# Kernel tuning notes

Measured on AMD Instinct MI355X. Metric: run time of the kernel, lower is better.

The kernel has to match this reference:

```python
import jax, jax.numpy as jnp
import numpy as np

IN_NC = 512

def setup_inputs() -> dict:
    key = jax.random.key(0)
    k1, k2, k3, k4 = jax.random.split(key, 4)
    B, N = 8, 2048
    nd, out_nc = 512, 512
    x = jax.random.normal(k1, (B, N * IN_NC), dtype=jnp.float32)
    # store weights as [in_nc, d] so projection is x @ W (same math as torch Linear with W^T)
    Wq = jax.random.normal(k2, (IN_NC, nd), dtype=jnp.float32) * (1.0 / np.sqrt(IN_NC))
    Wk = jax.random.normal(k3, (IN_NC, nd), dtype=jnp.float32) * (1.0 / np.sqrt(IN_NC))
    Wv = jax.random.normal(k4, (IN_NC, out_nc), dtype=jnp.float32) * (1.0 / np.sqrt(IN_NC))
    return {"x": x, "Wq": Wq, "Wk": Wk, "Wv": Wv}

def reference(x, Wq, Wk, Wv):
    B = x.shape[0]
    N = x.shape[1] // IN_NC
    xt = x.reshape(B, N, IN_NC)                     # [B, N, in_nc]
    Q = jnp.einsum('bnc,cd->bnd', xt, Wq)           # [B, N, nd]
    K = jnp.einsum('bnc,cd->bnd', xt, Wk)           # [B, N, nd]
    V = jnp.einsum('bnc,cd->bnd', xt, Wv)           # [B, N, out_nc]
    A = jnp.einsum('bnd,bmd->bnm', Q, K)            # [B, N, N]  (no scale, as in source)
    A = jax.nn.softmax(A, axis=-1)
    out = jnp.einsum('bnm,bmd->bnd', A, V)          # [B, N, out_nc]
    return out.reshape(B, -1)
```

## Files before the change

### kernel.cpp

```cpp
#include <hip/hip_runtime.h>
#include <hip/hip_fp16.h>

typedef _Float16 f16x8 __attribute__((ext_vector_type(8)));
typedef _Float16 f16x4 __attribute__((ext_vector_type(4)));
typedef float    f32x4 __attribute__((ext_vector_type(4)));

#define LOG2E 1.44269504f

__device__ __forceinline__ void stage128x64(const _Float16* __restrict__ g, int ld,
                                            void* lds, int tid)
{
    const int r0   = tid >> 3;
    const int colh = ((tid & 7) ^ (r0 & 7)) << 3;
    char* lbase = (char*)lds + (tid >> 6) * 1024;
#pragma unroll
    for (int i = 0; i < 4; i++) {
        const _Float16* src = g + (size_t)(i * 32 + r0) * ld + colh;
        __builtin_amdgcn_global_load_lds(
            (const __attribute__((address_space(1))) void*)src,
            (__attribute__((address_space(3))) void*)(lbase + i * 4096),
            16, 0, 0);
    }
}

__device__ __forceinline__ f16x8 lds_frag(const void* lds, int row, int colh)
{
    const int off = row * 128 + ((colh * 2) ^ ((row & 7) << 4));
    return *(const f16x8*)((const char*)lds + off);
}

__device__ __forceinline__ void mfma_tile(const void* a_lds, const void* b_lds,
                                          f32x4 acc[4][4],
                                          int wr, int wc, int lrow, int lkg)
{
#pragma unroll
    for (int kk = 0; kk < 2; kk++) {
        f16x8 af[4], bf[4];
#pragma unroll
        for (int mi = 0; mi < 4; mi++)
            af[mi] = lds_frag(a_lds, wr * 64 + mi * 16 + lrow, kk * 32 + lkg * 8);
#pragma unroll
        for (int ni = 0; ni < 4; ni++)
            bf[ni] = lds_frag(b_lds, wc * 64 + ni * 16 + lrow, kk * 32 + lkg * 8);
#pragma unroll
        for (int mi = 0; mi < 4; mi++)
#pragma unroll
            for (int ni = 0; ni < 4; ni++)
                acc[mi][ni] = __builtin_amdgcn_mfma_f32_16x16x32_f16(af[mi], bf[ni], acc[mi][ni], 0, 0, 0);
    }
}

__device__ __forceinline__ void gemm_loop_db(const _Float16* __restrict__ A, int lda,
                                             const _Float16* __restrict__ B, int ldb,
                                             int nk,
                                             _Float16* a0, _Float16* a1,
                                             _Float16* b0, _Float16* b1,
                                             f32x4 acc[4][4], int tid,
                                             int wr, int wc, int lrow, int lkg)
{
    stage128x64(A, lda, a0, tid);
    stage128x64(B, ldb, b0, tid);
    __syncthreads();
    for (int t = 0; t < nk; ++t) {
        _Float16* acur = (t & 1) ? a1 : a0;
        _Float16* bcur = (t & 1) ? b1 : b0;
        if (t + 1 < nk) {
            _Float16* anx = (t & 1) ? a0 : a1;
            _Float16* bnx = (t & 1) ? b0 : b1;
            stage128x64(A + (size_t)(t + 1) * 64, lda, anx, tid);
            stage128x64(B + (size_t)(t + 1) * 64, ldb, bnx, tid);
        }
        mfma_tile(acur, bcur, acc, wr, wc, lrow, lkg);
        __syncthreads();
    }
}

__global__ __launch_bounds__(256)
void convert_kernel(const float* __restrict__ x,
                    const float* __restrict__ Wq,
                    const float* __restrict__ Wk,
                    const float* __restrict__ Wv,
                    _Float16* __restrict__ xh,
                    _Float16* __restrict__ Wt)
{
    const int b = blockIdx.x;
    if (b < 2048) {
        const size_t base = (size_t)b * 4096 + (size_t)threadIdx.x * 4;
#pragma unroll
        for (int i = 0; i < 4; i++) {
            f32x4 v = *(const f32x4*)(x + base + i * 1024);
            f16x4 h;
#pragma unroll
            for (int j = 0; j < 4; j++) h[j] = (_Float16)v[j];
            *(f16x4*)(xh + base + i * 1024) = h;
        }
    } else {
        __shared__ float tb[32][33];
        const int t = b - 2048;
        const int mat = t >> 8;
        const int tile = t & 255;
        const int tr = tile >> 4, tc = tile & 15;
        const float* W = (mat == 0) ? Wq : (mat == 1) ? Wk : Wv;
        const int r = threadIdx.x >> 5, c = threadIdx.x & 31;
#pragma unroll
        for (int p = 0; p < 4; p++)
            tb[p * 8 + r][c] = W[(size_t)(tr * 32 + p * 8 + r) * 512 + tc * 32 + c];
        __syncthreads();
#pragma unroll
        for (int p = 0; p < 4; p++)
            Wt[((size_t)mat * 512 + tc * 32 + p * 8 + r) * 512 + tr * 32 + c] =
                (_Float16)tb[c][p * 8 + r];
    }
}

__global__ __launch_bounds__(256)
void proj_kernel(const _Float16* __restrict__ xh,
                 const _Float16* __restrict__ Wt,
                 _Float16* __restrict__ Qf,
                 _Float16* __restrict__ Kf,
                 _Float16* __restrict__ Vt)
{
    __shared__ _Float16 a0[128 * 64], a1[128 * 64];
    __shared__ _Float16 b0[128 * 64], b1[128 * 64];

    const int tid = threadIdx.x;
    const int mb = blockIdx.x, cb = blockIdx.y;
    const int mat = cb >> 2, nb = cb & 3;
    const int m0 = mb * 128, n0 = nb * 128;

    const _Float16* Abase = xh + (size_t)m0 * 512;
    const _Float16* Bbase = Wt + ((size_t)mat * 512 + n0) * 512;

    const int lane = tid & 63;
    const int w = tid >> 6;
    const int wr = w >> 1, wc = w & 1;
    const int lrow = lane & 15, lkg = lane >> 4;

    f32x4 acc[4][4];
#pragma unroll
    for (int i = 0; i < 4; i++)
#pragma unroll
        for (int j = 0; j < 4; j++) acc[i][j] = (f32x4)0.0f;

    gemm_loop_db(Abase, 512, Bbase, 512, 8, a0, a1, b0, b1,
                 acc, tid, wr, wc, lrow, lkg);

    if (mat < 2) {
        _Float16* Out = (mat == 0) ? Qf : Kf;
#pragma unroll
        for (int mi = 0; mi < 4; mi++) {
            const int mbase = m0 + wr * 64 + mi * 16 + lkg * 4;
#pragma unroll
            for (int ni = 0; ni < 4; ni++) {
                const int ncol = n0 + wc * 64 + ni * 16 + lrow;
#pragma unroll
                for (int r = 0; r < 4; r++)
                    Out[(size_t)(mbase + r) * 512 + ncol] = (_Float16)acc[mi][ni][r];
            }
        }
    } else {
#pragma unroll
        for (int mi = 0; mi < 4; mi++) {
            const int mglob = m0 + wr * 64 + mi * 16 + lkg * 4;
            const int b = mglob >> 11, mloc = mglob & 2047;
#pragma unroll
            for (int ni = 0; ni < 4; ni++) {
                const int d = n0 + wc * 64 + ni * 16 + lrow;
                f16x4 h;
#pragma unroll
                for (int r = 0; r < 4; r++) h[r] = (_Float16)acc[mi][ni][r];
                *(f16x4*)&Vt[((size_t)b * 512 + d) * 2048 + mloc] = h;
            }
        }
    }
}

__global__ __launch_bounds__(256)
void score_kernel(const _Float16* __restrict__ Qf,
                  const _Float16* __restrict__ Kf,
                  _Float16* __restrict__ P,
                  float2* __restrict__ ML, int b0)
{
    __shared__ __align__(16) char smem[65536];
    _Float16* a0 = (_Float16*)smem;
    _Float16* a1 = (_Float16*)(smem + 16384);
    _Float16* b0p = (_Float16*)(smem + 32768);
    _Float16* b1p = (_Float16*)(smem + 49152);
    float (*S_lds)[132] = (float(*)[132])smem;

    const int tid = threadIdx.x;
    const int mb = blockIdx.x, nb = blockIdx.y, bl = blockIdx.z;
    const int bg = b0 + bl;

    const _Float16* Abase = Qf + (size_t)(bg * 2048 + nb * 128) * 512;
    const _Float16* Bbase = Kf + (size_t)(bg * 2048 + mb * 128) * 512;

    const int lane = tid & 63;
    const int w = tid >> 6;
    const int wr = w >> 1, wc = w & 1;
    const int lrow = lane & 15, lkg = lane >> 4;

    f32x4 acc[4][4];
#pragma unroll
    for (int i = 0; i < 4; i++)
#pragma unroll
        for (int j = 0; j < 4; j++) acc[i][j] = (f32x4)0.0f;

    gemm_loop_db(Abase, 512, Bbase, 512, 8, a0, a1, b0p, b1p,
                 acc, tid, wr, wc, lrow, lkg);

    _Float16* Pb = P + (size_t)bl * 2048 * 2048;
    const int s  = tid >> 2;
    const int c0 = (tid & 3) * 32;

#pragma unroll
    for (int hp = 0; hp < 2; hp++) {
#pragma unroll
        for (int m2 = 0; m2 < 2; m2++) {
            const int mi = hp * 2 + m2;
            const int srow = wr * 32 + m2 * 16 + lkg * 4;
#pragma unroll
            for (int ni = 0; ni < 4; ni++) {
                const int col = wc * 64 + ni * 16 + lrow;
#pragma unroll
                for (int rr = 0; rr < 4; rr++)
                    S_lds[srow + rr][col] = acc[mi][ni][rr];
            }
        }
        __syncthreads();

        f32x4 vv[8];
#pragma unroll
        for (int j = 0; j < 8; j++)
            vv[j] = *(const f32x4*)&S_lds[s][c0 + j * 4];

        float m = vv[0][0];
#pragma unroll
        for (int j = 0; j < 8; j++)
#pragma unroll
            for (int jj = 0; jj < 4; jj++) m = fmaxf(m, vv[j][jj]);
        m = fmaxf(m, __shfl_xor(m, 1));
        m = fmaxf(m, __shfl_xor(m, 2));

        float l = 0.0f;
#pragma unroll
        for (int j = 0; j < 8; j++)
#pragma unroll
            for (int jj = 0; jj < 4; jj++) {
                float e = exp2f((vv[j][jj] - m) * LOG2E);
                vv[j][jj] = e;
                l += e;
            }
        l += __shfl_xor(l, 1);
        l += __shfl_xor(l, 2);

        const int q_local = (s >> 5) * 64 + hp * 32 + (s & 31);
        const int q = nb * 128 + q_local;

        if ((tid & 3) == 0) {
            float2 v; v.x = m; v.y = l;
            ML[((size_t)bl * 2048 + q) * 16 + mb] = v;
        }

#pragma unroll
        for (int j = 0; j < 4; j++) {
            f16x8 h;
#pragma unroll
            for (int jj = 0; jj < 8; jj++) {
                const int idx = j * 8 + jj;
                h[jj] = (_Float16)vv[idx >> 2][idx & 3];
            }
            *(f16x8*)&Pb[(size_t)q * 2048 + mb * 128 + c0 + j * 8] = h;
        }
        __syncthreads();
    }
}

__global__ __launch_bounds__(256)
void out_kernel(const _Float16* __restrict__ P,
                const _Float16* __restrict__ Vt,
                const float2* __restrict__ ML,
                float* __restrict__ out, int b0)
{
    __shared__ _Float16 a0[128 * 64], a1[128 * 64];
    __shared__ _Float16 b0p[128 * 64], b1p[128 * 64];
    __shared__ float scale_lds[128][17];

    const int tid = threadIdx.x;
    const int db = blockIdx.x >> 4, nb = blockIdx.x & 15, bl = blockIdx.y;
    const int bg = b0 + bl;

    if (tid < 128) {
        const float2* mlrow = ML + ((size_t)bl * 2048 + nb * 128 + tid) * 16;
        float2 ml[16];
        float M = -3.4e38f;
#pragma unroll
        for (int t = 0; t < 16; t++) { ml[t] = mlrow[t]; M = fmaxf(M, ml[t].x); }
        float L = 0.0f;
#pragma unroll
        for (int t = 0; t < 16; t++) L += ml[t].y * exp2f((ml[t].x - M) * LOG2E);
        const float invL = 1.0f / L;
#pragma unroll
        for (int t = 0; t < 16; t++)
            scale_lds[tid][t] = exp2f((ml[t].x - M) * LOG2E) * invL;
    }

    const _Float16* Abase = P  + (size_t)bl * 2048 * 2048 + (size_t)(nb * 128) * 2048;
    const _Float16* Bbase = Vt + (size_t)bg * 512  * 2048 + (size_t)(db * 128) * 2048;

    const int lane = tid & 63;
    const int w = tid >> 6;
    const int wr = w >> 1, wc = w & 1;
    const int lrow = lane & 15, lkg = lane >> 4;

    f32x4 acc[4][4];
#pragma unroll
    for (int i = 0; i < 4; i++)
#pragma unroll
        for (int j = 0; j < 4; j++) acc[i][j] = (f32x4)0.0f;

    stage128x64(Abase, 2048, a0, tid);
    stage128x64(Bbase, 2048, b0p, tid);
    __syncthreads();

    for (int t = 0; t < 32; ++t) {
        _Float16* acur = (t & 1) ? a1 : a0;
        _Float16* bcur = (t & 1) ? b1p : b0p;
        if (t + 1 < 32) {
            _Float16* anx = (t & 1) ? a0 : a1;
            _Float16* bnx = (t & 1) ? b0p : b1p;
            stage128x64(Abase + (size_t)(t + 1) * 64, 2048, anx, tid);
            stage128x64(Bbase + (size_t)(t + 1) * 64, 2048, bnx, tid);
        }
        const int kt = t >> 1;
#pragma unroll
        for (int kk = 0; kk < 2; kk++) {
            f16x8 af[4], bf[4];
#pragma unroll
            for (int mi = 0; mi < 4; mi++) {
                af[mi] = lds_frag(acur, wr * 64 + mi * 16 + lrow, kk * 32 + lkg * 8);
                const _Float16 hs = (_Float16)scale_lds[wr * 64 + mi * 16 + lrow][kt];
                af[mi] *= hs;
            }
#pragma unroll
            for (int ni = 0; ni < 4; ni++)
                bf[ni] = lds_frag(bcur, wc * 64 + ni * 16 + lrow, kk * 32 + lkg * 8);
#pragma unroll
            for (int mi = 0; mi < 4; mi++)
#pragma unroll
                for (int ni = 0; ni < 4; ni++)
                    acc[mi][ni] = __builtin_amdgcn_mfma_f32_16x16x32_f16(af[mi], bf[ni], acc[mi][ni], 0, 0, 0);
        }
        __syncthreads();
    }

#pragma unroll
    for (int mi = 0; mi < 4; mi++) {
        const int nbase = nb * 128 + wr * 64 + mi * 16 + lkg * 4;
#pragma unroll
        for (int ni = 0; ni < 4; ni++) {
            const int d = db * 128 + wc * 64 + ni * 16 + lrow;
#pragma unroll
            for (int rr = 0; rr < 4; rr++)
                out[((size_t)bg * 2048 + nbase + rr) * 512 + d] = acc[mi][ni][rr];
        }
    }
}

extern "C" void kernel_launch(void* const* d_in, const int* in_sizes, int n_in,
                              void* d_out, int out_size, void* d_ws, size_t ws_size,
                              hipStream_t stream) {
    const float* x  = (const float*)d_in[0];
    const float* Wq = (const float*)d_in[1];
    const float* Wk = (const float*)d_in[2];
    const float* Wv = (const float*)d_in[3];

    const size_t MB = 1024ull * 1024ull;
    char* ws = (char*)d_ws;
    _Float16* Qf = (_Float16*)ws;
    _Float16* Kf = Qf + (size_t)16384 * 512;
    _Float16* Vt = Kf + (size_t)16384 * 512;
    _Float16* P  = Vt + (size_t)16384 * 512;
    float*    out = (float*)d_out;

    int chunk;
    if      (ws_size >= 120 * MB) chunk = 8;
    else if (ws_size >= 88  * MB) chunk = 4;
    else if (ws_size >= 70  * MB) chunk = 2;
    else                          chunk = 1;

    float2* ML = (float2*)(P + (size_t)chunk * 2048 * 2048);

    _Float16* xh = (_Float16*)P;
    _Float16* Wt = xh + (size_t)16384 * 512;

    convert_kernel<<<2816, 256, 0, stream>>>(x, Wq, Wk, Wv, xh, Wt);
    proj_kernel<<<dim3(128, 12), 256, 0, stream>>>(xh, Wt, Qf, Kf, Vt);

    for (int b0 = 0; b0 < 8; b0 += chunk) {
        score_kernel<<<dim3(16, 16, chunk), 256, 0, stream>>>(Qf, Kf, P, ML, b0);
        out_kernel<<<dim3(64, chunk), 256, 0, stream>>>(P, Vt, ML, out, b0);
    }
}
```

Measured before the change: 159.2 us.

## Restructure GEMM main loops into prefetch-depth-two pipeline with explicit waitcnt barriers

Replaces the double-buffered GEMM loop in the proj, score and out kernels with a schedule that prefetches two K-tiles ahead. Each iteration loads all LDS fragments into registers, waits with an explicit lgkmcnt, hits a barrier, then reuses the just-consumed buffer for the tile two steps ahead. MFMAs run under raised priority, and partial vmcnt waits replace full __syncthreads so global loads overlap compute. The change also adds launch_bounds occupancy hints of 2 blocks per CU. It risks register pressure from holding both k-halves of fragments, and correctness depends on the hand-counted vmcnt values.

New measurement: 142.0 us. 10.8% less time.

```diff
diff --git a/kernel.cpp b/kernel.cpp
--- a/kernel.cpp
+++ b/kernel.cpp
@@ -29,30 +29,9 @@
     return *(const f16x8*)((const char*)lds + off);
 }
 
-__device__ __forceinline__ void mfma_tile(const void* a_lds, const void* b_lds,
-                                          f32x4 acc[4][4],
-                                          int wr, int wc, int lrow, int lkg)
-{
-#pragma unroll
-    for (int kk = 0; kk < 2; kk++) {
-        f16x8 af[4], bf[4];
-#pragma unroll
-        for (int mi = 0; mi < 4; mi++)
-            af[mi] = lds_frag(a_lds, wr * 64 + mi * 16 + lrow, kk * 32 + lkg * 8);
-#pragma unroll
-        for (int ni = 0; ni < 4; ni++)
-            bf[ni] = lds_frag(b_lds, wc * 64 + ni * 16 + lrow, kk * 32 + lkg * 8);
-#pragma unroll
-        for (int mi = 0; mi < 4; mi++)
-#pragma unroll
-            for (int ni = 0; ni < 4; ni++)
-                acc[mi][ni] = __builtin_amdgcn_mfma_f32_16x16x32_f16(af[mi], bf[ni], acc[mi][ni], 0, 0, 0);
-    }
-}
-
-__device__ __forceinline__ void gemm_loop_db(const _Float16* __restrict__ A, int lda,
+template<int NK>
+__device__ __forceinline__ void gemm_loop_cv(const _Float16* __restrict__ A, int lda,
                                              const _Float16* __restrict__ B, int ldb,
-                                             int nk,
                                              _Float16* a0, _Float16* a1,
                                              _Float16* b0, _Float16* b1,
                                              f32x4 acc[4][4], int tid,
@@ -60,18 +39,52 @@
 {
     stage128x64(A, lda, a0, tid);
     stage128x64(B, ldb, b0, tid);
-    __syncthreads();
-    for (int t = 0; t < nk; ++t) {
+    stage128x64(A + 64, lda, a1, tid);
+    stage128x64(B + 64, ldb, b1, tid);
+    asm volatile("s_waitcnt vmcnt(8)" ::: "memory");
+    __builtin_amdgcn_s_barrier();
+    __builtin_amdgcn_sched_barrier(0);
+
+    for (int t = 0; t < NK; ++t) {
         _Float16* acur = (t & 1) ? a1 : a0;
         _Float16* bcur = (t & 1) ? b1 : b0;
-        if (t + 1 < nk) {
-            _Float16* anx = (t & 1) ? a0 : a1;
-            _Float16* bnx = (t & 1) ? b0 : b1;
-            stage128x64(A + (size_t)(t + 1) * 64, lda, anx, tid);
-            stage128x64(B + (size_t)(t + 1) * 64, ldb, bnx, tid);
-        }
-        mfma_tile(acur, bcur, acc, wr, wc, lrow, lkg);
-        __syncthreads();
+
+        f16x8 af[2][4], bf[2][4];
+#pragma unroll
+        for (int kk = 0; kk < 2; kk++) {
+#pragma unroll
+            for (int mi = 0; mi < 4; mi++)
+                af[kk][mi] = lds_frag(acur, wr * 64 + mi * 16 + lrow, kk * 32 + lkg * 8);
+#pragma unroll
+            for (int ni = 0; ni < 4; ni++)
+                bf[kk][ni] = lds_frag(bcur, wc * 64 + ni * 16 + lrow, kk * 32 + lkg * 8);
+        }
+        asm volatile("s_waitcnt lgkmcnt(0)" ::: "memory");
+        __builtin_amdgcn_sched_barrier(0);
+        __builtin_amdgcn_s_barrier();
+
+        if (t + 2 < NK) {
+            stage128x64(A + (size_t)(t + 2) * 64, lda, acur, tid);
+            stage128x64(B + (size_t)(t + 2) * 64, ldb, bcur, tid);
+        }
+        __builtin_amdgcn_sched_barrier(0);
+
+        __builtin_amdgcn_s_setprio(1);
+#pragma unroll
+        for (int kk = 0; kk < 2; kk++)
+#pragma unroll
+            for (int mi = 0; mi < 4; mi++)
+#pragma unroll
+                for (int ni = 0; ni < 4; ni++)
+                    acc[mi][ni] = __builtin_amdgcn_mfma_f32_16x16x32_f16(
+                        af[kk][mi], bf[kk][ni], acc[mi][ni], 0, 0, 0);
+        __builtin_amdgcn_s_setprio(0);
+
+        if (t + 2 < NK) asm volatile("s_waitcnt vmcnt(8)" ::: "memory");
+        else            asm volatile("s_waitcnt vmcnt(0)" ::: "memory");
+        __builtin_amdgcn_sched_barrier(0);
+        __builtin_amdgcn_s_barrier();
+        __builtin_amdgcn_sched_barrier(0);
     }
 }
 
@@ -113,7 +126,7 @@
     }
 }
 
-__global__ __launch_bounds__(256)
+__global__ __launch_bounds__(256, 2)
 void proj_kernel(const _Float16* __restrict__ xh,
                  const _Float16* __restrict__ Wt,
                  _Float16* __restrict__ Qf,
@@ -142,8 +155,8 @@
 #pragma unroll
         for (int j = 0; j < 4; j++) acc[i][j] = (f32x4)0.0f;
 
-    gemm_loop_db(Abase, 512, Bbase, 512, 8, a0, a1, b0, b1,
-                 acc, tid, wr, wc, lrow, lkg);
+    gemm_loop_cv<8>(Abase, 512, Bbase, 512, a0, a1, b0, b1,
+                    acc, tid, wr, wc, lrow, lkg);
 
     if (mat < 2) {
         _Float16* Out = (mat == 0) ? Qf : Kf;
@@ -175,15 +188,15 @@
     }
 }
 
-__global__ __launch_bounds__(256)
+__global__ __launch_bounds__(256, 2)
 void score_kernel(const _Float16* __restrict__ Qf,
                   const _Float16* __restrict__ Kf,
                   _Float16* __restrict__ P,
                   float2* __restrict__ ML, int b0)
 {
     __shared__ __align__(16) char smem[65536];
-    _Float16* a0 = (_Float16*)smem;
-    _Float16* a1 = (_Float16*)(smem + 16384);
+    _Float16* a0  = (_Float16*)smem;
+    _Float16* a1  = (_Float16*)(smem + 16384);
     _Float16* b0p = (_Float16*)(smem + 32768);
     _Float16* b1p = (_Float16*)(smem + 49152);
     float (*S_lds)[132] = (float(*)[132])smem;
@@ -206,8 +219,8 @@
 #pragma unroll
         for (int j = 0; j < 4; j++) acc[i][j] = (f32x4)0.0f;
 
-    gemm_loop_db(Abase, 512, Bbase, 512, 8, a0, a1, b0p, b1p,
-                 acc, tid, wr, wc, lrow, lkg);
+    gemm_loop_cv<8>(Abase, 512, Bbase, 512, a0, a1, b0p, b1p,
+                    acc, tid, wr, wc, lrow, lkg);
 
     _Float16* Pb = P + (size_t)bl * 2048 * 2048;
     const int s  = tid >> 2;
@@ -276,7 +289,7 @@
     }
 }
 
-__global__ __launch_bounds__(256)
+__global__ __launch_bounds__(256, 2)
 void out_kernel(const _Float16* __restrict__ P,
                 const _Float16* __restrict__ Vt,
                 const float2* __restrict__ ML,
@@ -319,39 +332,63 @@
 #pragma unroll
         for (int j = 0; j < 4; j++) acc[i][j] = (f32x4)0.0f;
 
-    stage128x64(Abase, 2048, a0, tid);
-    stage128x64(Bbase, 2048, b0p, tid);
     __syncthreads();
+
+    stage128x64(Abase,      2048, a0,  tid);
+    stage128x64(Bbase,      2048, b0p, tid);
+    stage128x64(Abase + 64, 2048, a1,  tid);
+    stage128x64(Bbase + 64, 2048, b1p, tid);
+    asm volatile("s_waitcnt vmcnt(8)" ::: "memory");
+    __builtin_amdgcn_s_barrier();
+    __builtin_amdgcn_sched_barrier(0);
 
     for (int t = 0; t < 32; ++t) {
         _Float16* acur = (t & 1) ? a1 : a0;
         _Float16* bcur = (t & 1) ? b1p : b0p;
-        if (t + 1 < 32) {
-            _Float16* anx = (t & 1) ? a0 : a1;
-            _Float16* bnx = (t & 1) ? b0p : b1p;
-            stage128x64(Abase + (size_t)(t + 1) * 64, 2048, anx, tid);
-            stage128x64(Bbase + (size_t)(t + 1) * 64, 2048, bnx, tid);
-        }
         const int kt = t >> 1;
+
+        f16x8 af[2][4], bf[2][4];
+        float sc[4];
 #pragma unroll
         for (int kk = 0; kk < 2; kk++) {
-            f16x8 af[4], bf[4];
+#pragma unroll
+            for (int mi = 0; mi < 4; mi++)
+                af[kk][mi] = lds_frag(acur, wr * 64 + mi * 16 + lrow, kk * 32 + lkg * 8);
+#pragma unroll
+            for (int ni = 0; ni < 4; ni++)
+                bf[kk][ni] = lds_frag(bcur, wc * 64 + ni * 16 + lrow, kk * 32 + lkg * 8);
+        }
+#pragma unroll
+        for (int mi = 0; mi < 4; mi++)
+            sc[mi] = scale_lds[wr * 64 + mi * 16 + lrow][kt];
+        asm volatile("s_waitcnt lgkmcnt(0)" ::: "memory");
+        __builtin_amdgcn_sched_barrier(0);
+        __builtin_amdgcn_s_barrier();
+
+        if (t + 2 < 32) {
+            stage128x64(Abase + (size_t)(t + 2) * 64, 2048, acur, tid);
+            stage128x64(Bbase + (size_t)(t + 2) * 64, 2048, bcur, tid);
+        }
+        __builtin_amdgcn_sched_barrier(0);
+
+        __builtin_amdgcn_s_setprio(1);
+#pragma unroll
+        for (int kk = 0; kk < 2; kk++)
 #pragma unroll
             for (int mi = 0; mi < 4; mi++) {
-                af[mi] = lds_frag(acur, wr * 64 + mi * 16 + lrow, kk * 32 + lkg * 8);
-                const _Float16 hs = (_Float16)scale_lds[wr * 64 + mi * 16 + lrow][kt];
-                af[mi] *= hs;
-            }
-#pragma unroll
-            for (int ni = 0; ni < 4; ni++)
-                bf[ni] = lds_frag(bcur, wc * 64 + ni * 16 + lrow, kk * 32 + lkg * 8);
-#pragma unroll
-            for (int mi = 0; mi < 4; mi++)
+                const f16x8 a = af[kk][mi] * (_Float16)sc[mi];
 #pragma unroll
                 for (int ni = 0; ni < 4; ni++)
-                    acc[mi][ni] = __builtin_amdgcn_mfma_f32_16x16x32_f16(af[mi], bf[ni], acc[mi][ni], 0, 0, 0);
-        }
-        __syncthreads();
+                    acc[mi][ni] = __builtin_amdgcn_mfma_f32_16x16x32_f16(
+                        a, bf[kk][ni], acc[mi][ni], 0, 0, 0);
+            }
+        __builtin_amdgcn_s_setprio(0);
+
+        if (t + 2 < 32) asm volatile("s_waitcnt vmcnt(8)" ::: "memory");
+        else            asm volatile("s_waitcnt vmcnt(0)" ::: "memory");
+        __builtin_amdgcn_sched_barrier(0);
+        __builtin_amdgcn_s_barrier();
+        __builtin_amdgcn_sched_barrier(0);
     }
 
 #pragma unroll
```
